# Kernel optimization log

Measured on AMD Instinct MI355X. Metric: run time of the kernel, lower is better.

Reference implementation:

```python
import jax, jax.numpy as jnp
import numpy as np

IMG_H, IMG_W = 512, 512
FEAT_HW = [64, 32, 16, 8, 4]
STRIDES = [8, 16, 32, 64, 128]
IN_CH = 256
NUM_ANCHORS = 9
NUM_CLASSES = 91
SCORE_THRESH = 0.05
NMS_THRESH = 0.5
TOPK = 1000            # batch_size_per_image
DETS = 300             # detections_per_image
BBOX_CLIP = float(np.log(1000.0 / 16.0))
PRIOR_P = 0.01


def _make_anchors():
    # torchvision-style grid anchors, 3 scales x 3 aspect ratios per location
    all_a = []
    for lvl, (hw, stride) in enumerate(zip(FEAT_HW, STRIDES)):
        base = 32.0 * (2.0 ** lvl)
        scales = np.array([1.0, 2.0 ** (1.0 / 3.0), 2.0 ** (2.0 / 3.0)])
        ratios = np.array([0.5, 1.0, 2.0])
        ws = (base * scales[None, :] / np.sqrt(ratios)[:, None]).reshape(-1)  # [9]
        hs = (base * scales[None, :] * np.sqrt(ratios)[:, None]).reshape(-1)
        shifts = (np.arange(hw) + 0.5) * stride
        cy, cx = np.meshgrid(shifts, shifts, indexing='ij')
        cx = cx.reshape(-1, 1)
        cy = cy.reshape(-1, 1)
        a = np.stack([cx - ws / 2, cy - hs / 2, cx + ws / 2, cy + hs / 2], axis=-1)  # [HW, 9, 4]
        all_a.append(a.reshape(-1, 4))
    return np.concatenate(all_a, axis=0).astype(np.float32)


def setup_inputs() -> dict:
    key = jax.random.key(0)
    ks = jax.random.split(key, 10)
    inp = {}
    for i, hw in enumerate(FEAT_HW):
        inp[f'feat{i}'] = jax.random.normal(ks[i], (1, IN_CH, hw, hw), jnp.float32)
    inp['anchors'] = jnp.asarray(_make_anchors())
    tower_std, out_std = 0.03, 0.01
    inp['cls_tower_w'] = jax.random.normal(ks[5], (4, IN_CH, IN_CH, 3, 3), jnp.float32) * tower_std
    inp['cls_tower_b'] = jnp.zeros((4, IN_CH), jnp.float32)
    inp['cls_logits_w'] = jax.random.normal(ks[6], (NUM_ANCHORS * NUM_CLASSES, IN_CH, 3, 3), jnp.float32) * out_std
    inp['cls_logits_b'] = jnp.full((NUM_ANCHORS * NUM_CLASSES,), -np.log((1.0 - PRIOR_P) / PRIOR_P), jnp.float32)
    inp['reg_tower_w'] = jax.random.normal(ks[7], (4, IN_CH, IN_CH, 3, 3), jnp.float32) * tower_std
    inp['reg_tower_b'] = jnp.zeros((4, IN_CH), jnp.float32)
    inp['reg_bbox_w'] = jax.random.normal(ks[8], (NUM_ANCHORS * 4, IN_CH, 3, 3), jnp.float32) * out_std
    inp['reg_bbox_b'] = jnp.zeros((NUM_ANCHORS * 4,), jnp.float32)
    return inp


def _conv3x3(x, w, b):
    y = jax.lax.conv_general_dilated(x, w, (1, 1), 'SAME', dimension_numbers=('NCHW', 'OIHW', 'NCHW'))
    return y + b[None, :, None, None]


def _head(x, tw, tb, ow, ob, out_ch):
    # 4-layer conv tower with ReLU, then output conv; reshape to [B, H*W*A, out_ch]
    for i in range(4):
        x = jax.nn.relu(_conv3x3(x, tw[i], tb[i]))
    y = _conv3x3(x, ow, ob)  # [B, A*out_ch, H, W]
    B, _, H, W = y.shape
    return y.reshape(B, NUM_ANCHORS, out_ch, H, W).transpose(0, 3, 4, 1, 2).reshape(B, H * W * NUM_ANCHORS, out_ch)


def _decode(rel, anc):
    # BoxCoder.decode_single with weights (1,1,1,1)
    w = anc[:, 2] - anc[:, 0]
    h = anc[:, 3] - anc[:, 1]
    cx = anc[:, 0] + 0.5 * w
    cy = anc[:, 1] + 0.5 * h
    dx, dy = rel[:, 0], rel[:, 1]
    dw = jnp.minimum(rel[:, 2], BBOX_CLIP)
    dh = jnp.minimum(rel[:, 3], BBOX_CLIP)
    pcx = dx * w + cx
    pcy = dy * h + cy
    pw = jnp.exp(dw) * w
    ph = jnp.exp(dh) * h
    return jnp.stack([pcx - 0.5 * pw, pcy - 0.5 * ph, pcx + 0.5 * pw, pcy + 0.5 * ph], axis=1)


def _level_candidates(logits, reg, anc):
    # logits [A_l, K], reg [A_l, 4], anc [A_l, 4]
    scores = jax.nn.sigmoid(logits).reshape(-1)          # [A_l*K]
    masked = jnp.where(scores > SCORE_THRESH, scores, -1.0)
    top_s, top_i = jax.lax.top_k(masked, TOPK)           # fixed-size topk; invalid -> -1
    labels = top_i % NUM_CLASSES
    a_idx = top_i // NUM_CLASSES
    boxes = _decode(reg[a_idx], anc[a_idx])
    boxes = jnp.stack([
        jnp.clip(boxes[:, 0], 0.0, float(IMG_W)), jnp.clip(boxes[:, 1], 0.0, float(IMG_H)),
        jnp.clip(boxes[:, 2], 0.0, float(IMG_W)), jnp.clip(boxes[:, 3], 0.0, float(IMG_H))], axis=1)
    return top_s, boxes, labels


def _nms_image(boxes, scores, labels):
    # batched_nms: offset boxes by label so different classes never overlap,
    # then greedy NMS with fixed DETS iterations (padded with invalid slots).
    NEG = jnp.float32(-1e9)
    off = labels.astype(boxes.dtype) * (jnp.max(boxes) + 1.0)
    b = boxes + off[:, None]
    area = (b[:, 2] - b[:, 0]) * (b[:, 3] - b[:, 1])
    alive0 = jnp.where(scores > SCORE_THRESH, scores, NEG)

    def step(alive, _):
        j = jnp.argmax(alive)
        valid = alive[j] > SCORE_THRESH
        bj = b[j]
        lt = jnp.maximum(bj[:2], b[:, :2])
        rb = jnp.minimum(bj[2:], b[:, 2:])
        wh = jnp.maximum(rb - lt, 0.0)
        inter = wh[:, 0] * wh[:, 1]
        iou = inter / (area[j] + area - inter + 1e-12)
        alive = jnp.where(iou > NMS_THRESH, NEG, alive).at[j].set(NEG)
        return alive, (j, valid)

    _, (sel, valid) = jax.lax.scan(step, alive0, None, length=DETS)
    out_s = jnp.where(valid, scores[sel], 0.0)
    out_b = jnp.where(valid[:, None], boxes[sel], 0.0)
    out_l = jnp.where(valid, labels[sel], -1)
    return out_s, out_b, out_l


def _forward(feats, anchors, ctw, ctb, cow, cob, rtw, rtb, row, rob):
    cand = []
    a_off = 0
    for f in feats:
        B, _, H, W = f.shape
        logits = _head(f, ctw, ctb, cow, cob, NUM_CLASSES)   # [B, HWA, K]
        reg = _head(f, rtw, rtb, row, rob, 4)                # [B, HWA, 4]
        a_l = H * W * NUM_ANCHORS
        anc = anchors[a_off:a_off + a_l]
        a_off += a_l
        cand.append(jax.vmap(_level_candidates, in_axes=(0, 0, None))(logits, reg, anc))
    scores = jnp.concatenate([c[0] for c in cand], axis=1)   # [B, 5*TOPK]
    boxes = jnp.concatenate([c[1] for c in cand], axis=1)    # [B, 5*TOPK, 4]
    labels = jnp.concatenate([c[2] for c in cand], axis=1)
    out_s, out_b, out_l = jax.vmap(_nms_image)(boxes, scores, labels)
    out = jnp.concatenate([out_s[..., None], out_b], axis=-1)  # [B, DETS, 5] = (score, x1, y1, x2, y2)
    return out, out_l


def reference(feat0, feat1, feat2, feat3, feat4, anchors, cls_tower_w, cls_tower_b,
              cls_logits_w, cls_logits_b, reg_tower_w, reg_tower_b, reg_bbox_w, reg_bbox_b):
    out, labels = _forward([feat0, feat1, feat2, feat3, feat4], anchors,
                           cls_tower_w, cls_tower_b, cls_logits_w, cls_logits_b,
                           reg_tower_w, reg_tower_b, reg_bbox_w, reg_bbox_b)
    return out, labels
```

## Files before the change

kernel.cpp:

```cpp
#include <hip/hip_runtime.h>
#include <hip/hip_bf16.h>
#include <math.h>

#define CIN 256
#define NUM_CLASSES 91
#define NUM_ANCH 9
#define KEY_CAP 65536
#define NCAND 5000
#define BBOX_CLIP_F 4.135166556742356f
#define CLS_THRESH 0.05f
#define PITCH 5456
#define PP_TOT 5972
#define PLANE_E 1528832
#define PLANE_B 3057664
#define ABUF_B  6115328
#define SLB     147456
#define LO_OFF  13312
#define PHASE   26624

typedef __attribute__((ext_vector_type(4))) float f4;
typedef _Float16 h8 __attribute__((ext_vector_type(8)));

#define MFMA(a,b,c) __builtin_amdgcn_mfma_f32_16x16x32_f16(a,b,c,0,0,0)

__constant__ int c_wsh[5]  = {6,5,4,3,2};
__constant__ int c_hw[5]   = {4096,1024,256,64,16};
__constant__ int c_wp[5]   = {66,34,18,10,6};
__constant__ int c_poff[5] = {0,4356,5512,5836,5936};
__constant__ int c_slen[5] = {198,136,108,100,36};
__constant__ int c_loff[5] = {0,4096,5120,5376,5440};
__constant__ int c_aoff[5] = {0,36864,46080,48384,48960};
__constant__ int s_cum[11] = {0,16,32,48,64,80,96,112,164,168,184};

__device__ __forceinline__ unsigned short f16r(float f) {
    _Float16 h = (_Float16)f;
    return __builtin_bit_cast(unsigned short, h);
}
__device__ __forceinline__ float f16tof(unsigned short u) {
    return (float)__builtin_bit_cast(_Float16, u);
}
__device__ __forceinline__ void split16(float v, unsigned short& h, unsigned short& l) {
    unsigned short hh = (fabsf(v) < 6.103515625e-05f) ? (unsigned short)0 : f16r(v);
    h = hh;
    l = f16r((v - f16tof(hh)) * 4096.0f);
}
__device__ __forceinline__ void gl_lds(const void* g, void* l) {
    __builtin_amdgcn_global_load_lds((const __attribute__((address_space(1))) void*)g,
                                     (__attribute__((address_space(3))) void*)l, 16, 0, 0);
}
__device__ __forceinline__ void tile_geom(int tile, int& lvl, int& px0, int& y0) {
    if (tile < 64)      { lvl = 0; px0 = tile << 6; y0 = tile; }
    else if (tile < 80) { lvl = 1; int j = tile - 64; px0 = j << 6; y0 = j << 1; }
    else if (tile < 84) { lvl = 2; int j = tile - 80; px0 = j << 6; y0 = j << 2; }
    else if (tile == 84){ lvl = 3; px0 = 0; y0 = 0; }
    else                { lvl = 4; px0 = 0; y0 = 0; }
}

__global__ void pad_k(const float* __restrict__ f0, const float* __restrict__ f1,
                      const float* __restrict__ f2, const float* __restrict__ f3,
                      const float* __restrict__ f4, unsigned short* __restrict__ IN) {
    int gid = blockIdx.x * 256 + threadIdx.x;
    if (gid >= 256 * PITCH) return;
    int cin = gid / PITCH, g = gid - cin * PITCH;
    int lvl = (g < 4096) ? 0 : (g < 5120) ? 1 : (g < 5376) ? 2 : (g < 5440) ? 3 : 4;
    const float* f = (lvl == 0) ? f0 : (lvl == 1) ? f1 : (lvl == 2) ? f2 : (lvl == 3) ? f3 : f4;
    int pix = g - c_loff[lvl];
    int wsh = c_wsh[lvl];
    int y = pix >> wsh, x = pix & ((1 << wsh) - 1);
    float v = f[(size_t)cin * c_hw[lvl] + pix];
    unsigned short h, l;
    split16(v, h, l);
    size_t idx = ((size_t)(cin >> 5) * PP_TOT + c_poff[lvl] + (size_t)(y + 1) * c_wp[lvl] + x + 1) * 32 + (cin & 31);
    IN[idx] = h;
    IN[PLANE_E + idx] = l;
}

__global__ void wprep_k(const float* __restrict__ ctw, const float* __restrict__ rtw,
                        const float* __restrict__ cow, const float* __restrict__ row_,
                        unsigned short* __restrict__ wf) {
    int gid = blockIdx.x * 256 + threadIdx.x;
    if (gid >= 184 * 72 * 64) return;
    int lane = gid & 63;
    int t = gid >> 6;
    int tap = t % 9;
    int t2 = t / 9;
    int chunk = t2 & 7;
    int cbg = t2 >> 3;
    int r = 0;
#pragma unroll
    for (int i = 1; i <= 10; ++i) if (cbg >= s_cum[i]) r = i;
    int cbl = cbg - s_cum[r];
    const float* src;
    int coutCnt;
    if (r < 3)       { src = ctw + (size_t)(r + 1) * 589824; coutCnt = 256; }
    else if (r < 7)  { src = rtw + (size_t)(r - 3) * 589824; coutCnt = 256; }
    else if (r == 7) { src = cow; coutCnt = 819; }
    else if (r == 8) { src = row_; coutCnt = 36; }
    else             { src = ctw; coutCnt = 256; }
    int cout = cbl * 16 + (lane & 15);
    int q = lane >> 4;
    unsigned short H[8], L[8];
#pragma unroll
    for (int j = 0; j < 8; ++j) {
        int cin = chunk * 32 + q * 8 + j;
        float v = (cout < coutCnt) ? src[((size_t)cout * 256 + cin) * 9 + tap] : 0.0f;
        split16(v, H[j], L[j]);
    }
    size_t off = (size_t)cbg * 73728 + (size_t)(chunk * 9 + tap) * 1024 + (size_t)lane * 8;
#pragma unroll
    for (int j = 0; j < 8; ++j) { wf[off + j] = H[j]; wf[off + 512 + j] = L[j]; }
}

__device__ __forceinline__ void kloop(const unsigned short* __restrict__ src,
        const char* __restrict__ wf0, char* sm, int wid, int lane,
        int s_base, int s_len, int Wp, const int sloc[2], f4 acc1[2][4], f4 acc2[2][4]) {
    const char* wp = wf0 + lane * 16;
    int nc = (s_len * 64 + 1023) >> 10;
    const char* gbase = (const char*)src;
    {
        const char* g = gbase + (size_t)s_base * 64;
        for (int c = wid; c < nc; c += 4) {
            gl_lds(g + (size_t)c * 1024 + (size_t)lane * 16, sm + c * 1024);
            gl_lds(g + PLANE_B + (size_t)c * 1024 + (size_t)lane * 16, sm + LO_OFF + c * 1024);
        }
    }
    __syncthreads();
    for (int chunk = 0; chunk < 8; ++chunk) {
        char* smc = sm + (chunk & 1) * PHASE;
        if (chunk < 7) {
            char* smn = sm + ((chunk & 1) ^ 1) * PHASE;
            const char* g = gbase + ((size_t)(chunk + 1) * PP_TOT + s_base) * 64;
            for (int c = wid; c < nc; c += 4) {
                gl_lds(g + (size_t)c * 1024 + (size_t)lane * 16, smn + c * 1024);
                gl_lds(g + PLANE_B + (size_t)c * 1024 + (size_t)lane * 16, smn + LO_OFF + c * 1024);
            }
        }
#pragma unroll
        for (int tap = 0; tap < 9; ++tap) {
            int toff = ((tap / 3) - 1) * Wp + (tap % 3) - 1;
            int so = toff * 64;
            int wo = (chunk * 9 + tap) * 2048;
            h8 ah0 = *(const h8*)(smc + sloc[0] + so);
            h8 al0 = *(const h8*)(smc + LO_OFF + sloc[0] + so);
            h8 ah1 = *(const h8*)(smc + sloc[1] + so);
            h8 al1 = *(const h8*)(smc + LO_OFF + sloc[1] + so);
#pragma unroll
            for (int sl = 0; sl < 4; ++sl) {
                h8 bh = *(const h8*)(wp + (size_t)sl * SLB + wo);
                h8 bl = *(const h8*)(wp + (size_t)sl * SLB + wo + 1024);
                acc1[0][sl] = MFMA(ah0, bh, acc1[0][sl]);
                acc2[0][sl] = MFMA(al0, bh, acc2[0][sl]);
                acc2[0][sl] = MFMA(ah0, bl, acc2[0][sl]);
                acc1[1][sl] = MFMA(ah1, bh, acc1[1][sl]);
                acc2[1][sl] = MFMA(al1, bh, acc2[1][sl]);
                acc2[1][sl] = MFMA(ah1, bl, acc2[1][sl]);
            }
        }
        __syncthreads();
    }
}

__global__ __launch_bounds__(256, 3) void conv_t(
        const unsigned short* __restrict__ srcC, const unsigned short* __restrict__ srcR,
        unsigned short* __restrict__ dstC, unsigned short* __restrict__ dstR,
        const unsigned short* __restrict__ wfC, const unsigned short* __restrict__ wfR,
        const float* __restrict__ bC, const float* __restrict__ bR) {
    __shared__ __align__(16) char sm[2 * PHASE];
    int tid = threadIdx.x, lane = tid & 63, wid = tid >> 6;
    int quad = lane >> 4, l16 = lane & 15;
    int bx = blockIdx.x, tile = bx >> 2, rem = bx & 3;
    int tower = rem >> 1, cb = rem & 1;
    const unsigned short* src = tower ? srcR : srcC;
    unsigned short* dst = tower ? dstR : dstC;
    const unsigned short* wfx = tower ? wfR : wfC;
    const float* bias = tower ? bR : bC;

    int lvl, px0, y0;
    tile_geom(tile, lvl, px0, y0);
    int wsh = c_wsh[lvl], HW = c_hw[lvl], Wp = c_wp[lvl];
    int poff = c_poff[lvl];
    int s_base = poff + y0 * Wp, s_len = c_slen[lvl];
    int Mh = (wid & 1) * 32, Nh64 = wid >> 1;

    int sloc[2];
#pragma unroll
    for (int mb = 0; mb < 2; ++mb) {
        int p = px0 + Mh + mb * 16 + l16;
        if (p >= HW) p = HW - 1;
        int y = p >> wsh, x = p & ((1 << wsh) - 1);
        sloc[mb] = ((y - y0 + 1) * Wp + x + 1) * 64 + quad * 16;
    }
    f4 acc1[2][4], acc2[2][4];
#pragma unroll
    for (int mb = 0; mb < 2; ++mb)
#pragma unroll
        for (int sl = 0; sl < 4; ++sl) { acc1[mb][sl] = (f4)0.0f; acc2[mb][sl] = (f4)0.0f; }

    const char* wf0 = (const char*)wfx + (size_t)(cb * 8 + Nh64 * 4) * SLB;
    kloop(src, wf0, sm, wid, lane, s_base, s_len, Wp, sloc, acc1, acc2);

    int cbase = cb * 128 + Nh64 * 64;
    float bv[4];
#pragma unroll
    for (int sl = 0; sl < 4; ++sl) bv[sl] = bias[cbase + sl * 16 + l16];
#pragma unroll
    for (int mb = 0; mb < 2; ++mb) {
        int pb = px0 + Mh + mb * 16 + quad * 4;
#pragma unroll
        for (int r = 0; r < 4; ++r) {
            int p = pb + r;
            bool valid = p < HW;
            int pc = valid ? p : 0;
            int y = pc >> wsh, x = pc & ((1 << wsh) - 1);
            size_t ppix = poff + (size_t)(y + 1) * Wp + x + 1;
#pragma unroll
            for (int sl = 0; sl < 4; ++sl) {
                int coutg = cbase + sl * 16 + l16;
                float v = fmaf(acc2[mb][sl][r], 0.000244140625f, acc1[mb][sl][r]) + bv[sl];
                v = fmaxf(v, 0.0f);
                unsigned short h, l;
                split16(v, h, l);
                size_t idx = ((size_t)(coutg >> 5) * PP_TOT + ppix) * 32 + (coutg & 31);
                if (valid) { dst[idx] = h; dst[PLANE_E + idx] = l; }
            }
        }
    }
}

__global__ __launch_bounds__(256, 3) void mhead_t(
        const unsigned short* __restrict__ srcC, const unsigned short* __restrict__ srcR,
        const unsigned short* __restrict__ wfCls, const unsigned short* __restrict__ wfReg,
        const float* __restrict__ cob, const float* __restrict__ rob,
        unsigned long long* __restrict__ keys, int* __restrict__ cnt,
        float* __restrict__ regout) {
    __shared__ __align__(16) char sm[2 * PHASE];
    int tid = threadIdx.x, lane = tid & 63, wid = tid >> 6;
    int quad = lane >> 4, l16 = lane & 15;
    int bx = blockIdx.x, tile = bx >> 3, sub = bx & 7;
    bool isCls = sub < 7;

    int lvl, px0, y0;
    tile_geom(tile, lvl, px0, y0);
    int wsh = c_wsh[lvl], HW = c_hw[lvl], Wp = c_wp[lvl];
    int poff = c_poff[lvl];
    int s_base = poff + y0 * Wp, s_len = c_slen[lvl];
    int Mh = (wid & 1) * 32, Nh64 = wid >> 1;

    int sloc[2];
#pragma unroll
    for (int mb = 0; mb < 2; ++mb) {
        int p = px0 + Mh + mb * 16 + l16;
        if (p >= HW) p = HW - 1;
        int y = p >> wsh, x = p & ((1 << wsh) - 1);
        sloc[mb] = ((y - y0 + 1) * Wp + x + 1) * 64 + quad * 16;
    }
    f4 acc1[2][4], acc2[2][4];
#pragma unroll
    for (int mb = 0; mb < 2; ++mb)
#pragma unroll
        for (int sl = 0; sl < 4; ++sl) { acc1[mb][sl] = (f4)0.0f; acc2[mb][sl] = (f4)0.0f; }

    const unsigned short* src = isCls ? srcC : srcR;
    const char* wf0 = isCls ? (const char*)wfCls + (size_t)(sub * 8 + Nh64 * 4) * SLB
                            : (const char*)wfReg + (size_t)(Nh64 * 4) * SLB;
    kloop(src, wf0, sm, wid, lane, s_base, s_len, Wp, sloc, acc1, acc2);

    if (isCls) {
        int chb = sub * 128 + Nh64 * 64;
        float cbv[4];
#pragma unroll
        for (int sl = 0; sl < 4; ++sl) {
            int ch = chb + sl * 16 + l16;
            cbv[sl] = (ch < 819) ? cob[ch] : 0.0f;
        }
#pragma unroll
        for (int mb = 0; mb < 2; ++mb) {
            int pb = px0 + Mh + mb * 16 + quad * 4;
#pragma unroll
            for (int r = 0; r < 4; ++r) {
                int p = pb + r;
                bool valid = p < HW;
#pragma unroll
                for (int sl = 0; sl < 4; ++sl) {
                    int ch = chb + sl * 16 + l16;
                    if (valid && ch < 819) {
                        float lg = fmaf(acc2[mb][sl][r], 0.000244140625f, acc1[mb][sl][r]) + cbv[sl];
                        float s = 1.0f / (1.0f + expf(-lg));
                        if (s > CLS_THRESH) {
                            int a = ch / NUM_CLASSES;
                            int cls = ch - a * NUM_CLASSES;
                            unsigned flat = (unsigned)((p * NUM_ANCH + a) * NUM_CLASSES + cls);
                            int pos = atomicAdd(cnt + lvl, 1);
                            if (pos < KEY_CAP)
                                keys[(size_t)lvl * KEY_CAP + pos] =
                                    ((unsigned long long)__float_as_uint(s) << 32) |
                                    (unsigned long long)(~flat);
                        }
                    }
                }
            }
        }
    } else {
        int chb = Nh64 * 64;
        float rbv[4];
#pragma unroll
        for (int sl = 0; sl < 4; ++sl) {
            int ch = chb + sl * 16 + l16;
            rbv[sl] = (ch < 36) ? rob[ch] : 0.0f;
        }
        int loff = c_loff[lvl];
#pragma unroll
        for (int mb = 0; mb < 2; ++mb) {
            int pb = px0 + Mh + mb * 16 + quad * 4;
#pragma unroll
            for (int r = 0; r < 4; ++r) {
                int p = pb + r;
                bool valid = p < HW;
#pragma unroll
                for (int sl = 0; sl < 4; ++sl) {
                    int ch = chb + sl * 16 + l16;
                    if (valid && ch < 36)
                        regout[(size_t)ch * PITCH + loff + p] =
                            fmaf(acc2[mb][sl][r], 0.000244140625f, acc1[mb][sl][r]) + rbv[sl];
                }
            }
        }
    }
}

__global__ __launch_bounds__(1024) void sort5_k(unsigned long long* keys, const int* cnt) {
    const int lvl = blockIdx.x;
    unsigned long long* kb = keys + (size_t)lvl * KEY_CAP;
    int n = cnt[lvl]; if (n > KEY_CAP) n = KEY_CAP;
    int m = 2; while (m < n) m <<= 1;
    __shared__ unsigned long long sk[8192];
    if (m <= 8192) {
        for (int i = threadIdx.x; i < m; i += 1024) sk[i] = (i < n) ? kb[i] : 0ull;
        __syncthreads();
        for (int k = 2; k <= m; k <<= 1)
            for (int j = k >> 1; j > 0; j >>= 1) {
                for (int i = threadIdx.x; i < m; i += 1024) {
                    int ixj = i ^ j;
                    if (ixj > i) {
                        unsigned long long a = sk[i], b = sk[ixj];
                        bool desc = (i & k) == 0;
                        if (desc ? (a < b) : (a > b)) { sk[i] = b; sk[ixj] = a; }
                    }
                }
                __syncthreads();
            }
        for (int i = threadIdx.x; i < m; i += 1024) kb[i] = sk[i];
    } else {
        for (int i = threadIdx.x; i < m; i += 1024) if (i >= n) kb[i] = 0ull;
        __syncthreads();
        for (int k = 2; k <= m; k <<= 1)
            for (int j = k >> 1; j > 0; j >>= 1) {
                for (int i = threadIdx.x; i < m; i += 1024) {
                    int ixj = i ^ j;
                    if (ixj > i) {
                        unsigned long long a = kb[i], b = kb[ixj];
                        bool desc = (i & k) == 0;
                        if (desc ? (a < b) : (a > b)) { kb[i] = b; kb[ixj] = a; }
                    }
                }
                __syncthreads();
            }
    }
}

__global__ void emit_k(const unsigned long long* __restrict__ keys, const int* __restrict__ cnt,
                       const float* __restrict__ regout, const float* __restrict__ anchors,
                       float* __restrict__ cs, float* __restrict__ cb, int* __restrict__ cl) {
#pragma clang fp contract(off)
    int r = blockIdx.x * 256 + threadIdx.x;
    if (r >= NCAND) return;
    int lvl = r / 1000, rr = r - lvl * 1000;
    int n = cnt[lvl]; if (n > KEY_CAP) n = KEY_CAP; if (n > 1000) n = 1000;
    float score = -1.0f, b0 = 0.f, b1 = 0.f, b2 = 0.f, b3 = 0.f;
    int label = 0;
    if (rr < n) {
        unsigned long long key = keys[(size_t)lvl * KEY_CAP + rr];
        score = __uint_as_float((unsigned)(key >> 32));
        unsigned flat = ~((unsigned)(key & 0xFFFFFFFFull));
        label = (int)(flat % NUM_CLASSES);
        int af = (int)(flat / NUM_CLASSES);
        int a = af % NUM_ANCH;
        int pix = af / NUM_ANCH;
        int gp = c_loff[lvl] + pix;
        float dx = regout[(size_t)(a * 4 + 0) * PITCH + gp];
        float dy = regout[(size_t)(a * 4 + 1) * PITCH + gp];
        float dw = regout[(size_t)(a * 4 + 2) * PITCH + gp];
        float dh = regout[(size_t)(a * 4 + 3) * PITCH + gp];
        const float* an = anchors + (size_t)(c_aoff[lvl] + af) * 4;
        float aw = an[2] - an[0];
        float ah = an[3] - an[1];
        float cx = an[0] + 0.5f * aw;
        float cy = an[1] + 0.5f * ah;
        dw = fminf(dw, BBOX_CLIP_F);
        dh = fminf(dh, BBOX_CLIP_F);
        float pcx = dx * aw + cx;
        float pcy = dy * ah + cy;
        float pw = expf(dw) * aw;
        float ph = expf(dh) * ah;
        b0 = fminf(fmaxf(pcx - 0.5f * pw, 0.0f), 512.0f);
        b1 = fminf(fmaxf(pcy - 0.5f * ph, 0.0f), 512.0f);
        b2 = fminf(fmaxf(pcx + 0.5f * pw, 0.0f), 512.0f);
        b3 = fminf(fmaxf(pcy + 0.5f * ph, 0.0f), 512.0f);
    }
    cs[r] = score;
    cb[(size_t)r * 4 + 0] = b0;
    cb[(size_t)r * 4 + 1] = b1;
    cb[(size_t)r * 4 + 2] = b2;
    cb[(size_t)r * 4 + 3] = b3;
    cl[r] = label;
}

__global__ void rank_k(const float* __restrict__ cs, const float* __restrict__ cbx,
                       const int* __restrict__ cl, const int* __restrict__ cnt,
                       int* __restrict__ order, float* __restrict__ sbox,
                       float* __restrict__ sarea, int* __restrict__ nvp) {
#pragma clang fp contract(off)
    __shared__ int vls[5];
    int t = blockIdx.x * 256 + threadIdx.x;
    if (threadIdx.x < 5) {
        int n = cnt[threadIdx.x]; if (n > 1000) n = 1000;
        vls[threadIdx.x] = n;
    }
    __syncthreads();
    if (t >= NCAND) return;
    if (t == 0) *nvp = vls[0] + vls[1] + vls[2] + vls[3] + vls[4];
    int lvl = t / 1000, pos = t - lvl * 1000;
    if (pos >= vls[lvl]) return;
    float s = cs[t];
    int rank = pos;
#pragma unroll
    for (int l2 = 0; l2 < 5; ++l2) {
        if (l2 == lvl) continue;
        int n = vls[l2];
        const float* seg = cs + l2 * 1000;
        int lo = 0, hi = n;
        if (l2 < lvl) {
            while (lo < hi) { int mid = (lo + hi) >> 1; if (seg[mid] >= s) lo = mid + 1; else hi = mid; }
        } else {
            while (lo < hi) { int mid = (lo + hi) >> 1; if (seg[mid] > s) lo = mid + 1; else hi = mid; }
        }
        rank += lo;
    }
    order[rank] = t;
    float off = (float)cl[t] * 513.0f;
    float x1 = cbx[(size_t)t * 4 + 0] + off;
    float y1 = cbx[(size_t)t * 4 + 1] + off;
    float x2 = cbx[(size_t)t * 4 + 2] + off;
    float y2 = cbx[(size_t)t * 4 + 3] + off;
    sbox[(size_t)rank * 4 + 0] = x1;
    sbox[(size_t)rank * 4 + 1] = y1;
    sbox[(size_t)rank * 4 + 2] = x2;
    sbox[(size_t)rank * 4 + 3] = y2;
    sarea[rank] = (x2 - x1) * (y2 - y1);
}

__global__ void mask_k(const float* __restrict__ sbox, const float* __restrict__ sarea,
                       const int* __restrict__ nvp, unsigned long long* __restrict__ mask) {
#pragma clang fp contract(off)
    int nv = *nvp;
    int t = blockIdx.x * 256 + threadIdx.x;
    if (t >= NCAND * 80) return;
    int i = t / 80, w = t - i * 80;
    if (i >= nv) return;
    float ix1 = sbox[(size_t)i * 4 + 0];
    float iy1 = sbox[(size_t)i * 4 + 1];
    float ix2 = sbox[(size_t)i * 4 + 2];
    float iy2 = sbox[(size_t)i * 4 + 3];
    float ai = sarea[i];
    unsigned long long bits = 0ull;
    int j0 = w * 64;
    for (int b = 0; b < 64; ++b) {
        int j = j0 + b;
        if (j < nv) {
            float jx1 = sbox[(size_t)j * 4 + 0];
            float jy1 = sbox[(size_t)j * 4 + 1];
            float jx2 = sbox[(size_t)j * 4 + 2];
            float jy2 = sbox[(size_t)j * 4 + 3];
            float aj = sarea[j];
            float ltx = fmaxf(ix1, jx1), lty = fmaxf(iy1, jy1);
            float rbx = fminf(ix2, jx2), rby = fminf(iy2, jy2);
            float wx = fmaxf(rbx - ltx, 0.0f), wy = fmaxf(rby - lty, 0.0f);
            float inter = wx * wy;
            float iou = inter / (ai + aj - inter + 1e-12f);
            if (iou > 0.5f) bits |= (1ull << b);
        }
    }
    mask[(size_t)i * 80 + w] = bits;
}

__global__ __launch_bounds__(64) void sweep_k(const unsigned long long* __restrict__ mask,
        const int* __restrict__ nvp, int* __restrict__ accbuf, int* __restrict__ naccp) {
    const int l = threadIdx.x;
    int nv = *nvp; if (nv > NCAND) nv = NCAND;
    int nacc = 0;
    if (nv > 0) {
        unsigned long long sup0 = 0ull, sup1 = 0ull;
        int ntiles = (nv + 63) >> 6;
        bool done = false;
        for (int g0 = 0; g0 < ntiles && !done; g0 += 8) {
            int gcnt = ntiles - g0; if (gcnt > 8) gcnt = 8;
            unsigned long long ml[8];
#pragma unroll
            for (int g = 0; g < 8; ++g) {
                int t = g0 + g;
                int row = (t << 6) + l;
                ml[g] = (g < gcnt && row < nv) ? mask[(size_t)row * 80 + t] : 0ull;
            }
            for (int g = 0; g < gcnt && !done; ++g) {
                int t = g0 + g;
                unsigned long long cur = (t < 64)
                    ? (unsigned long long)__shfl((long long)sup0, t, 64)
                    : (unsigned long long)__shfl((long long)sup1, t - 64, 64);
                int lim = nv - (t << 6);
                unsigned long long valid = (lim >= 64) ? ~0ull : ((1ull << lim) - 1ull);
                unsigned long long rem = ~cur & valid;
                unsigned long long Aset = 0ull;
                while (rem) {
                    int k = __builtin_ctzll(rem);
                    Aset |= 1ull << k;
                    if (l == 0) accbuf[nacc] = (t << 6) + k;
                    ++nacc;
                    if (nacc == 300) { done = true; break; }
                    unsigned long long mlk = (unsigned long long)__shfl((long long)ml[g], k, 64);
                    cur |= mlk | (1ull << k);
                    rem = ~cur & valid;
                }
                if (!done) {
                    unsigned long long t2 = Aset;
                    while (t2) {
                        int i0 = __builtin_ctzll(t2); t2 &= t2 - 1;
                        int i1 = -1, i2 = -1, i3 = -1;
                        if (t2) { i1 = __builtin_ctzll(t2); t2 &= t2 - 1; }
                        if (t2) { i2 = __builtin_ctzll(t2); t2 &= t2 - 1; }
                        if (t2) { i3 = __builtin_ctzll(t2); t2 &= t2 - 1; }
                        size_t r0 = (size_t)((t << 6) + i0) * 80;
                        unsigned long long w0 = mask[r0 + l];
                        unsigned long long w1 = (i1 >= 0) ? mask[(size_t)((t << 6) + i1) * 80 + l] : 0ull;
                        unsigned long long w2 = (i2 >= 0) ? mask[(size_t)((t << 6) + i2) * 80 + l] : 0ull;
                        unsigned long long w3 = (i3 >= 0) ? mask[(size_t)((t << 6) + i3) * 80 + l] : 0ull;
                        sup0 |= w0 | w1 | w2 | w3;
                        if (l < 16) {
                            unsigned long long v0 = mask[r0 + 64 + l];
                            unsigned long long v1 = (i1 >= 0) ? mask[(size_t)((t << 6) + i1) * 80 + 64 + l] : 0ull;
                            unsigned long long v2 = (i2 >= 0) ? mask[(size_t)((t << 6) + i2) * 80 + 64 + l] : 0ull;
                            unsigned long long v3 = (i3 >= 0) ? mask[(size_t)((t << 6) + i3) * 80 + 64 + l] : 0ull;
                            sup1 |= v0 | v1 | v2 | v3;
                        }
                    }
                }
            }
        }
    }
    if (l == 0) *naccp = nacc;
}

__global__ void fill_k(const float* __restrict__ cs, const float* __restrict__ cb,
                       const int* __restrict__ cl, const int* __restrict__ order,
                       const int* __restrict__ accbuf, const int* __restrict__ naccp,
                       float* __restrict__ out) {
    int t = blockIdx.x * 64 + threadIdx.x;
    if (t >= 300) return;
    int na = *naccp;
    if (t < na) {
        int c = order[accbuf[t]];
        out[t * 5 + 0] = cs[c];
        out[t * 5 + 1] = cb[(size_t)c * 4 + 0];
        out[t * 5 + 2] = cb[(size_t)c * 4 + 1];
        out[t * 5 + 3] = cb[(size_t)c * 4 + 2];
        out[t * 5 + 4] = cb[(size_t)c * 4 + 3];
        out[1500 + t] = (float)cl[c];
    } else {
        out[t * 5 + 0] = 0.0f; out[t * 5 + 1] = 0.0f; out[t * 5 + 2] = 0.0f;
        out[t * 5 + 3] = 0.0f; out[t * 5 + 4] = 0.0f;
        out[1500 + t] = -1.0f;
    }
}

extern "C" void kernel_launch(void* const* d_in, const int* in_sizes, int n_in,
                              void* d_out, int out_size, void* d_ws, size_t ws_size,
                              hipStream_t stream) {
    const float* f0 = (const float*)d_in[0];
    const float* f1 = (const float*)d_in[1];
    const float* f2 = (const float*)d_in[2];
    const float* f3 = (const float*)d_in[3];
    const float* f4 = (const float*)d_in[4];
    const float* anchors = (const float*)d_in[5];
    const float* ctw = (const float*)d_in[6];
    const float* ctb = (const float*)d_in[7];
    const float* cow = (const float*)d_in[8];
    const float* cob = (const float*)d_in[9];
    const float* rtw = (const float*)d_in[10];
    const float* rtb = (const float*)d_in[11];
    const float* row_ = (const float*)d_in[12];
    const float* rob = (const float*)d_in[13];
    float* out = (float*)d_out;

    char* base = (char*)d_ws;
    unsigned short* wf = (unsigned short*)base;
    unsigned short* C  = (unsigned short*)(base + 24772608);
    unsigned short* IN = (unsigned short*)(base + 30887936);
    unsigned short* A  = (unsigned short*)(base + 37003264);
    unsigned short* B  = (unsigned short*)(base + 43118592);
    int* cnt           = (int*)(base + 49233920);
    int* nvp           = cnt + 6;
    int* naccp         = cnt + 7;
    float* cs    = (float*)(base + 0);
    float* cbx   = (float*)(base + 32768);
    int*   cl    = (int*)(base + 131072);
    int*   order = (int*)(base + 163840);
    float* sbox  = (float*)(base + 262144);
    float* sarea = (float*)(base + 344064);
    int*   accbuf = (int*)(base + 368640);
    unsigned long long* keys = (unsigned long long*)A;
    float* regout            = (float*)(base + 37003264 + 2621440);
    unsigned long long* mask = (unsigned long long*)B;

    unsigned short* SL_clsL[4] = {wf + (size_t)168 * 73728, wf + (size_t)0 * 73728,
                                  wf + (size_t)16 * 73728,  wf + (size_t)32 * 73728};
    unsigned short* SL_regL[4] = {wf + (size_t)48 * 73728, wf + (size_t)64 * 73728,
                                  wf + (size_t)80 * 73728, wf + (size_t)96 * 73728};
    unsigned short* SL_clsH = wf + (size_t)112 * 73728;
    unsigned short* SL_regH = wf + (size_t)164 * 73728;

    hipMemsetAsync(C, 0, 4 * (size_t)ABUF_B, stream);
    hipMemsetAsync(cnt, 0, 32, stream);

    pad_k<<<(256 * PITCH + 255) / 256, 256, 0, stream>>>(f0, f1, f2, f3, f4, IN);
    wprep_k<<<(184 * 72 * 64 + 255) / 256, 256, 0, stream>>>(ctw, rtw, cow, row_, wf);

    conv_t<<<86 * 4, 256, 0, stream>>>(IN, IN, A, B, SL_clsL[0], SL_regL[0], ctb, rtb);
    hipMemsetAsync(C, 0, (size_t)ABUF_B, stream);
    conv_t<<<86 * 4, 256, 0, stream>>>(A, B, C, IN, SL_clsL[1], SL_regL[1], ctb + 256, rtb + 256);
    conv_t<<<86 * 4, 256, 0, stream>>>(C, IN, A, B, SL_clsL[2], SL_regL[2], ctb + 512, rtb + 512);
    conv_t<<<86 * 4, 256, 0, stream>>>(A, B, C, IN, SL_clsL[3], SL_regL[3], ctb + 768, rtb + 768);

    mhead_t<<<86 * 8, 256, 0, stream>>>(C, IN, SL_clsH, SL_regH, cob, rob, keys, cnt, regout);

    sort5_k<<<5, 1024, 0, stream>>>(keys, cnt);
    emit_k<<<(NCAND + 255) / 256, 256, 0, stream>>>(keys, cnt, regout, anchors, cs, cbx, cl);
    rank_k<<<(NCAND + 255) / 256, 256, 0, stream>>>(cs, cbx, cl, cnt, order, sbox, sarea, nvp);
    mask_k<<<(NCAND * 80 + 255) / 256, 256, 0, stream>>>(sbox, sarea, nvp, mask);
    sweep_k<<<1, 64, 0, stream>>>(mask, nvp, accbuf, naccp);
    fill_k<<<5, 64, 0, stream>>>(cs, cbx, cl, order, accbuf, naccp, out);
}
```

Before: 653.2 us.

## Halve output-channel tile per block, double grid, prefetch weight fragments across taps

Each conv and head block now covers 64 output channels instead of 128, with each wave holding 2 channel slices instead of 4. This doubles the conv grid and expands the head grid to 14 blocks per tile, which raises parallelism and cuts accumulator registers. The tap loop also software-pipelines the B-fragment global loads, issuing the next tap's weights before the current tap's MFMAs to hide latency. The cost is that every input tile is staged into LDS twice as often per output channel, which doubles activation traffic per unit of MFMA work.

After: 528.2 us. 1.24x faster.

```diff
diff --git a/kernel.cpp b/kernel.cpp
--- a/kernel.cpp
+++ b/kernel.cpp
@@ -113,7 +113,7 @@
 
 __device__ __forceinline__ void kloop(const unsigned short* __restrict__ src,
         const char* __restrict__ wf0, char* sm, int wid, int lane,
-        int s_base, int s_len, int Wp, const int sloc[2], f4 acc1[2][4], f4 acc2[2][4]) {
+        int s_base, int s_len, int Wp, const int sloc[2], f4 acc1[2][2], f4 acc2[2][2]) {
     const char* wp = wf0 + lane * 16;
     int nc = (s_len * 64 + 1023) >> 10;
     const char* gbase = (const char*)src;
@@ -124,6 +124,10 @@
             gl_lds(g + PLANE_B + (size_t)c * 1024 + (size_t)lane * 16, sm + LO_OFF + c * 1024);
         }
     }
+    h8 bh0 = *(const h8*)(wp);
+    h8 bl0 = *(const h8*)(wp + 1024);
+    h8 bh1 = *(const h8*)(wp + SLB);
+    h8 bl1 = *(const h8*)(wp + SLB + 1024);
     __syncthreads();
     for (int chunk = 0; chunk < 8; ++chunk) {
         char* smc = sm + (chunk & 1) * PHASE;
@@ -137,24 +141,31 @@
         }
 #pragma unroll
         for (int tap = 0; tap < 9; ++tap) {
+            int kt = chunk * 9 + tap;
+            int wo2 = ((kt < 71) ? kt + 1 : kt) * 2048;
+            h8 nh0 = *(const h8*)(wp + wo2);
+            h8 nl0 = *(const h8*)(wp + wo2 + 1024);
+            h8 nh1 = *(const h8*)(wp + SLB + wo2);
+            h8 nl1 = *(const h8*)(wp + SLB + wo2 + 1024);
             int toff = ((tap / 3) - 1) * Wp + (tap % 3) - 1;
             int so = toff * 64;
-            int wo = (chunk * 9 + tap) * 2048;
             h8 ah0 = *(const h8*)(smc + sloc[0] + so);
             h8 al0 = *(const h8*)(smc + LO_OFF + sloc[0] + so);
             h8 ah1 = *(const h8*)(smc + sloc[1] + so);
             h8 al1 = *(const h8*)(smc + LO_OFF + sloc[1] + so);
-#pragma unroll
-            for (int sl = 0; sl < 4; ++sl) {
-                h8 bh = *(const h8*)(wp + (size_t)sl * SLB + wo);
-                h8 bl = *(const h8*)(wp + (size_t)sl * SLB + wo + 1024);
-                acc1[0][sl] = MFMA(ah0, bh, acc1[0][sl]);
-                acc2[0][sl] = MFMA(al0, bh, acc2[0][sl]);
-                acc2[0][sl] = MFMA(ah0, bl, acc2[0][sl]);
-                acc1[1][sl] = MFMA(ah1, bh, acc1[1][sl]);
-                acc2[1][sl] = MFMA(al1, bh, acc2[1][sl]);
-                acc2[1][sl] = MFMA(ah1, bl, acc2[1][sl]);
-            }
+            acc1[0][0] = MFMA(ah0, bh0, acc1[0][0]);
+            acc2[0][0] = MFMA(al0, bh0, acc2[0][0]);
+            acc2[0][0] = MFMA(ah0, bl0, acc2[0][0]);
+            acc1[1][0] = MFMA(ah1, bh0, acc1[1][0]);
+            acc2[1][0] = MFMA(al1, bh0, acc2[1][0]);
+            acc2[1][0] = MFMA(ah1, bl0, acc2[1][0]);
+            acc1[0][1] = MFMA(ah0, bh1, acc1[0][1]);
+            acc2[0][1] = MFMA(al0, bh1, acc2[0][1]);
+            acc2[0][1] = MFMA(ah0, bl1, acc2[0][1]);
+            acc1[1][1] = MFMA(ah1, bh1, acc1[1][1]);
+            acc2[1][1] = MFMA(al1, bh1, acc2[1][1]);
+            acc2[1][1] = MFMA(ah1, bl1, acc2[1][1]);
+            bh0 = nh0; bl0 = nl0; bh1 = nh1; bl1 = nl1;
         }
         __syncthreads();
     }
@@ -168,8 +179,8 @@
     __shared__ __align__(16) char sm[2 * PHASE];
     int tid = threadIdx.x, lane = tid & 63, wid = tid >> 6;
     int quad = lane >> 4, l16 = lane & 15;
-    int bx = blockIdx.x, tile = bx >> 2, rem = bx & 3;
-    int tower = rem >> 1, cb = rem & 1;
+    int bx = blockIdx.x;
+    int cb = bx & 3, tower = (bx >> 2) & 1, tile = bx >> 3;
     const unsigned short* src = tower ? srcR : srcC;
     unsigned short* dst = tower ? dstR : dstC;
     const unsigned short* wfx = tower ? wfR : wfC;
@@ -180,7 +191,7 @@
     int wsh = c_wsh[lvl], HW = c_hw[lvl], Wp = c_wp[lvl];
     int poff = c_poff[lvl];
     int s_base = poff + y0 * Wp, s_len = c_slen[lvl];
-    int Mh = (wid & 1) * 32, Nh64 = wid >> 1;
+    int Mh = (wid & 1) * 32, Nh32 = wid >> 1;
 
     int sloc[2];
 #pragma unroll
@@ -190,19 +201,19 @@
         int y = p >> wsh, x = p & ((1 << wsh) - 1);
         sloc[mb] = ((y - y0 + 1) * Wp + x + 1) * 64 + quad * 16;
     }
-    f4 acc1[2][4], acc2[2][4];
+    f4 acc1[2][2], acc2[2][2];
 #pragma unroll
     for (int mb = 0; mb < 2; ++mb)
 #pragma unroll
-        for (int sl = 0; sl < 4; ++sl) { acc1[mb][sl] = (f4)0.0f; acc2[mb][sl] = (f4)0.0f; }
-
-    const char* wf0 = (const char*)wfx + (size_t)(cb * 8 + Nh64 * 4) * SLB;
+        for (int sl = 0; sl < 2; ++sl) { acc1[mb][sl] = (f4)0.0f; acc2[mb][sl] = (f4)0.0f; }
+
+    const char* wf0 = (const char*)wfx + (size_t)(cb * 4 + Nh32 * 2) * SLB;
     kloop(src, wf0, sm, wid, lane, s_base, s_len, Wp, sloc, acc1, acc2);
 
-    int cbase = cb * 128 + Nh64 * 64;
-    float bv[4];
-#pragma unroll
-    for (int sl = 0; sl < 4; ++sl) bv[sl] = bias[cbase + sl * 16 + l16];
+    int cbase = cb * 64 + Nh32 * 32;
+    float bv[2];
+    bv[0] = bias[cbase + l16];
+    bv[1] = bias[cbase + 16 + l16];
 #pragma unroll
     for (int mb = 0; mb < 2; ++mb) {
         int pb = px0 + Mh + mb * 16 + quad * 4;
@@ -214,7 +225,7 @@
             int y = pc >> wsh, x = pc & ((1 << wsh) - 1);
             size_t ppix = poff + (size_t)(y + 1) * Wp + x + 1;
 #pragma unroll
-            for (int sl = 0; sl < 4; ++sl) {
+            for (int sl = 0; sl < 2; ++sl) {
                 int coutg = cbase + sl * 16 + l16;
                 float v = fmaf(acc2[mb][sl][r], 0.000244140625f, acc1[mb][sl][r]) + bv[sl];
                 v = fmaxf(v, 0.0f);
@@ -236,15 +247,15 @@
     __shared__ __align__(16) char sm[2 * PHASE];
     int tid = threadIdx.x, lane = tid & 63, wid = tid >> 6;
     int quad = lane >> 4, l16 = lane & 15;
-    int bx = blockIdx.x, tile = bx >> 3, sub = bx & 7;
-    bool isCls = sub < 7;
+    int bx = blockIdx.x, tile = bx / 14, sub = bx - tile * 14;
+    bool isCls = sub < 13;
 
     int lvl, px0, y0;
     tile_geom(tile, lvl, px0, y0);
     int wsh = c_wsh[lvl], HW = c_hw[lvl], Wp = c_wp[lvl];
     int poff = c_poff[lvl];
     int s_base = poff + y0 * Wp, s_len = c_slen[lvl];
-    int Mh = (wid & 1) * 32, Nh64 = wid >> 1;
+    int Mh = (wid & 1) * 32, Nh32 = wid >> 1;
 
     int sloc[2];
 #pragma unroll
@@ -254,22 +265,22 @@
         int y = p >> wsh, x = p & ((1 << wsh) - 1);
         sloc[mb] = ((y - y0 + 1) * Wp + x + 1) * 64 + quad * 16;
     }
-    f4 acc1[2][4], acc2[2][4];
+    f4 acc1[2][2], acc2[2][2];
 #pragma unroll
     for (int mb = 0; mb < 2; ++mb)
 #pragma unroll
-        for (int sl = 0; sl < 4; ++sl) { acc1[mb][sl] = (f4)0.0f; acc2[mb][sl] = (f4)0.0f; }
+        for (int sl = 0; sl < 2; ++sl) { acc1[mb][sl] = (f4)0.0f; acc2[mb][sl] = (f4)0.0f; }
 
     const unsigned short* src = isCls ? srcC : srcR;
-    const char* wf0 = isCls ? (const char*)wfCls + (size_t)(sub * 8 + Nh64 * 4) * SLB
-                            : (const char*)wfReg + (size_t)(Nh64 * 4) * SLB;
+    const char* wf0 = isCls ? (const char*)wfCls + (size_t)(sub * 4 + Nh32 * 2) * SLB
+                            : (const char*)wfReg + (size_t)(Nh32 * 2) * SLB;
     kloop(src, wf0, sm, wid, lane, s_base, s_len, Wp, sloc, acc1, acc2);
 
     if (isCls) {
-        int chb = sub * 128 + Nh64 * 64;
-        float cbv[4];
-#pragma unroll
-        for (int sl = 0; sl < 4; ++sl) {
+        int chb = sub * 64 + Nh32 * 32;
+        float cbv[2];
+#pragma unroll
+        for (int sl = 0; sl < 2; ++sl) {
             int ch = chb + sl * 16 + l16;
             cbv[sl] = (ch < 819) ? cob[ch] : 0.0f;
         }
@@ -281,7 +292,7 @@
                 int p = pb + r;
                 bool valid = p < HW;
 #pragma unroll
-                for (int sl = 0; sl < 4; ++sl) {
+                for (int sl = 0; sl < 2; ++sl) {
                     int ch = chb + sl * 16 + l16;
                     if (valid && ch < 819) {
                         float lg = fmaf(acc2[mb][sl][r], 0.000244140625f, acc1[mb][sl][r]) + cbv[sl];
@@ -301,10 +312,10 @@
             }
         }
     } else {
-        int chb = Nh64 * 64;
-        float rbv[4];
-#pragma unroll
-        for (int sl = 0; sl < 4; ++sl) {
+        int chb = Nh32 * 32;
+        float rbv[2];
+#pragma unroll
+        for (int sl = 0; sl < 2; ++sl) {
             int ch = chb + sl * 16 + l16;
             rbv[sl] = (ch < 36) ? rob[ch] : 0.0f;
         }
@@ -317,7 +328,7 @@
                 int p = pb + r;
                 bool valid = p < HW;
 #pragma unroll
-                for (int sl = 0; sl < 4; ++sl) {
+                for (int sl = 0; sl < 2; ++sl) {
                     int ch = chb + sl * 16 + l16;
                     if (valid && ch < 36)
                         regout[(size_t)ch * PITCH + loff + p] =
@@ -633,13 +644,13 @@
     pad_k<<<(256 * PITCH + 255) / 256, 256, 0, stream>>>(f0, f1, f2, f3, f4, IN);
     wprep_k<<<(184 * 72 * 64 + 255) / 256, 256, 0, stream>>>(ctw, rtw, cow, row_, wf);
 
-    conv_t<<<86 * 4, 256, 0, stream>>>(IN, IN, A, B, SL_clsL[0], SL_regL[0], ctb, rtb);
+    conv_t<<<86 * 8, 256, 0, stream>>>(IN, IN, A, B, SL_clsL[0], SL_regL[0], ctb, rtb);
     hipMemsetAsync(C, 0, (size_t)ABUF_B, stream);
-    conv_t<<<86 * 4, 256, 0, stream>>>(A, B, C, IN, SL_clsL[1], SL_regL[1], ctb + 256, rtb + 256);
-    conv_t<<<86 * 4, 256, 0, stream>>>(C, IN, A, B, SL_clsL[2], SL_regL[2], ctb + 512, rtb + 512);
-    conv_t<<<86 * 4, 256, 0, stream>>>(A, B, C, IN, SL_clsL[3], SL_regL[3], ctb + 768, rtb + 768);
-
-    mhead_t<<<86 * 8, 256, 0, stream>>>(C, IN, SL_clsH, SL_regH, cob, rob, keys, cnt, regout);
+    conv_t<<<86 * 8, 256, 0, stream>>>(A, B, C, IN, SL_clsL[1], SL_regL[1], ctb + 256, rtb + 256);
+    conv_t<<<86 * 8, 256, 0, stream>>>(C, IN, A, B, SL_clsL[2], SL_regL[2], ctb + 512, rtb + 512);
+    conv_t<<<86 * 8, 256, 0, stream>>>(A, B, C, IN, SL_clsL[3], SL_regL[3], ctb + 768, rtb + 768);
+
+    mhead_t<<<86 * 14, 256, 0, stream>>>(C, IN, SL_clsH, SL_regH, cob, rob, keys, cnt, regout);
 
     sort5_k<<<5, 1024, 0, stream>>>(keys, cnt);
     emit_k<<<(NCAND + 255) / 256, 256, 0, stream>>>(keys, cnt, regout, anchors, cs, cbx, cl);
```

## Halve conv blocks to two waves, swizzle activation layout, prefetch weights

Applied to the files above, without the earlier changes.

Conv and head kernels now run 128-thread blocks, two waves each covering 32 pixels by 64 output channels. This doubles the grid, so each block handles 64 channels instead of 128. The activation layout in global and LDS memory gains an XOR swizzle of the 8-channel groups keyed on pixel index, meant to reduce LDS bank conflicts on the A-operand reads. Weight fragments are loaded one tap ahead in registers to hide global latency. The cost is that each activation tile is staged into LDS twice as often across blocks, and register pressure rises.

New measurement: 680.3 us. 1.04x slower.

```diff
diff --git a/kernel.cpp b/kernel.cpp
--- a/kernel.cpp
+++ b/kernel.cpp
@@ -70,7 +70,10 @@
     float v = f[(size_t)cin * c_hw[lvl] + pix];
     unsigned short h, l;
     split16(v, h, l);
-    size_t idx = ((size_t)(cin >> 5) * PP_TOT + c_poff[lvl] + (size_t)(y + 1) * c_wp[lvl] + x + 1) * 32 + (cin & 31);
+    size_t ppix = c_poff[lvl] + (size_t)(y + 1) * c_wp[lvl] + x + 1;
+    int qc = (cin >> 3) & 3;
+    size_t idx = ((size_t)(cin >> 5) * PP_TOT + ppix) * 32 +
+                 (size_t)((qc ^ ((int)ppix & 3)) << 3) + (cin & 7);
     IN[idx] = h;
     IN[PLANE_E + idx] = l;
 }
@@ -112,55 +115,73 @@
 }
 
 __device__ __forceinline__ void kloop(const unsigned short* __restrict__ src,
-        const char* __restrict__ wf0, char* sm, int wid, int lane,
-        int s_base, int s_len, int Wp, const int sloc[2], f4 acc1[2][4], f4 acc2[2][4]) {
+        const char* __restrict__ wf0, char* sm, int wid, int lane, int quad,
+        int s_base, int s_len, int Wp, const int relrow[2], f4 acc1[2][4], f4 acc2[2][4]) {
     const char* wp = wf0 + lane * 16;
     int nc = (s_len * 64 + 1023) >> 10;
     const char* gbase = (const char*)src;
     {
         const char* g = gbase + (size_t)s_base * 64;
-        for (int c = wid; c < nc; c += 4) {
+        for (int c = wid; c < nc; c += 2) {
             gl_lds(g + (size_t)c * 1024 + (size_t)lane * 16, sm + c * 1024);
             gl_lds(g + PLANE_B + (size_t)c * 1024 + (size_t)lane * 16, sm + LO_OFF + c * 1024);
         }
     }
+    h8 bh[4], bl[4];
+#pragma unroll
+    for (int sl = 0; sl < 4; ++sl) {
+        bh[sl] = *(const h8*)(wp + (size_t)sl * SLB);
+        bl[sl] = *(const h8*)(wp + (size_t)sl * SLB + 1024);
+    }
     __syncthreads();
+    int qsh = quad << 4;
     for (int chunk = 0; chunk < 8; ++chunk) {
         char* smc = sm + (chunk & 1) * PHASE;
         if (chunk < 7) {
             char* smn = sm + ((chunk & 1) ^ 1) * PHASE;
             const char* g = gbase + ((size_t)(chunk + 1) * PP_TOT + s_base) * 64;
-            for (int c = wid; c < nc; c += 4) {
+            for (int c = wid; c < nc; c += 2) {
                 gl_lds(g + (size_t)c * 1024 + (size_t)lane * 16, smn + c * 1024);
                 gl_lds(g + PLANE_B + (size_t)c * 1024 + (size_t)lane * 16, smn + LO_OFF + c * 1024);
             }
         }
 #pragma unroll
         for (int tap = 0; tap < 9; ++tap) {
+            int kt = chunk * 9 + tap;
+            int wo2 = ((kt < 71) ? kt + 1 : kt) * 2048;
+            h8 nh[4], nl[4];
+#pragma unroll
+            for (int sl = 0; sl < 4; ++sl) {
+                nh[sl] = *(const h8*)(wp + (size_t)sl * SLB + wo2);
+                nl[sl] = *(const h8*)(wp + (size_t)sl * SLB + wo2 + 1024);
+            }
             int toff = ((tap / 3) - 1) * Wp + (tap % 3) - 1;
-            int so = toff * 64;
-            int wo = (chunk * 9 + tap) * 2048;
-            h8 ah0 = *(const h8*)(smc + sloc[0] + so);
-            h8 al0 = *(const h8*)(smc + LO_OFF + sloc[0] + so);
-            h8 ah1 = *(const h8*)(smc + sloc[1] + so);
-            h8 al1 = *(const h8*)(smc + LO_OFF + sloc[1] + so);
+            h8 ah[2], al[2];
+#pragma unroll
+            for (int mb = 0; mb < 2; ++mb) {
+                int arow = relrow[mb] + toff;
+                int sw = qsh ^ (((s_base + arow) & 3) << 4);
+                int addr = arow * 64 + sw;
+                ah[mb] = *(const h8*)(smc + addr);
+                al[mb] = *(const h8*)(smc + LO_OFF + addr);
+            }
 #pragma unroll
             for (int sl = 0; sl < 4; ++sl) {
-                h8 bh = *(const h8*)(wp + (size_t)sl * SLB + wo);
-                h8 bl = *(const h8*)(wp + (size_t)sl * SLB + wo + 1024);
-                acc1[0][sl] = MFMA(ah0, bh, acc1[0][sl]);
-                acc2[0][sl] = MFMA(al0, bh, acc2[0][sl]);
-                acc2[0][sl] = MFMA(ah0, bl, acc2[0][sl]);
-                acc1[1][sl] = MFMA(ah1, bh, acc1[1][sl]);
-                acc2[1][sl] = MFMA(al1, bh, acc2[1][sl]);
-                acc2[1][sl] = MFMA(ah1, bl, acc2[1][sl]);
-            }
+                acc1[0][sl] = MFMA(ah[0], bh[sl], acc1[0][sl]);
+                acc2[0][sl] = MFMA(al[0], bh[sl], acc2[0][sl]);
+                acc2[0][sl] = MFMA(ah[0], bl[sl], acc2[0][sl]);
+                acc1[1][sl] = MFMA(ah[1], bh[sl], acc1[1][sl]);
+                acc2[1][sl] = MFMA(al[1], bh[sl], acc2[1][sl]);
+                acc2[1][sl] = MFMA(ah[1], bl[sl], acc2[1][sl]);
+            }
+#pragma unroll
+            for (int sl = 0; sl < 4; ++sl) { bh[sl] = nh[sl]; bl[sl] = nl[sl]; }
         }
         __syncthreads();
     }
 }
 
-__global__ __launch_bounds__(256, 3) void conv_t(
+__global__ __launch_bounds__(128, 2) void conv_t(
         const unsigned short* __restrict__ srcC, const unsigned short* __restrict__ srcR,
         unsigned short* __restrict__ dstC, unsigned short* __restrict__ dstR,
         const unsigned short* __restrict__ wfC, const unsigned short* __restrict__ wfR,
@@ -168,8 +189,8 @@
     __shared__ __align__(16) char sm[2 * PHASE];
     int tid = threadIdx.x, lane = tid & 63, wid = tid >> 6;
     int quad = lane >> 4, l16 = lane & 15;
-    int bx = blockIdx.x, tile = bx >> 2, rem = bx & 3;
-    int tower = rem >> 1, cb = rem & 1;
+    int bx = blockIdx.x;
+    int cb = bx & 3, tower = (bx >> 2) & 1, tile = bx >> 3;
     const unsigned short* src = tower ? srcR : srcC;
     unsigned short* dst = tower ? dstR : dstC;
     const unsigned short* wfx = tower ? wfR : wfC;
@@ -180,15 +201,15 @@
     int wsh = c_wsh[lvl], HW = c_hw[lvl], Wp = c_wp[lvl];
     int poff = c_poff[lvl];
     int s_base = poff + y0 * Wp, s_len = c_slen[lvl];
-    int Mh = (wid & 1) * 32, Nh64 = wid >> 1;
-
-    int sloc[2];
+    int Mh = wid * 32;
+
+    int relrow[2];
 #pragma unroll
     for (int mb = 0; mb < 2; ++mb) {
         int p = px0 + Mh + mb * 16 + l16;
         if (p >= HW) p = HW - 1;
         int y = p >> wsh, x = p & ((1 << wsh) - 1);
-        sloc[mb] = ((y - y0 + 1) * Wp + x + 1) * 64 + quad * 16;
+        relrow[mb] = (y - y0 + 1) * Wp + x + 1;
     }
     f4 acc1[2][4], acc2[2][4];
 #pragma unroll
@@ -196,10 +217,10 @@
 #pragma unroll
         for (int sl = 0; sl < 4; ++sl) { acc1[mb][sl] = (f4)0.0f; acc2[mb][sl] = (f4)0.0f; }
 
-    const char* wf0 = (const char*)wfx + (size_t)(cb * 8 + Nh64 * 4) * SLB;
-    kloop(src, wf0, sm, wid, lane, s_base, s_len, Wp, sloc, acc1, acc2);
-
-    int cbase = cb * 128 + Nh64 * 64;
+    const char* wf0 = (const char*)wfx + (size_t)(cb * 4) * SLB;
+    kloop(src, wf0, sm, wid, lane, quad, s_base, s_len, Wp, relrow, acc1, acc2);
+
+    int cbase = cb * 64;
     float bv[4];
 #pragma unroll
     for (int sl = 0; sl < 4; ++sl) bv[sl] = bias[cbase + sl * 16 + l16];
@@ -220,14 +241,16 @@
                 v = fmaxf(v, 0.0f);
                 unsigned short h, l;
                 split16(v, h, l);
-                size_t idx = ((size_t)(coutg >> 5) * PP_TOT + ppix) * 32 + (coutg & 31);
+                int c31 = coutg & 31;
+                size_t idx = ((size_t)(coutg >> 5) * PP_TOT + ppix) * 32 +
+                             (size_t)(((c31 >> 3) ^ ((int)ppix & 3)) << 3) + (c31 & 7);
                 if (valid) { dst[idx] = h; dst[PLANE_E + idx] = l; }
             }
         }
     }
 }
 
-__global__ __launch_bounds__(256, 3) void mhead_t(
+__global__ __launch_bounds__(128, 2) void mhead_t(
         const unsigned short* __restrict__ srcC, const unsigned short* __restrict__ srcR,
         const unsigned short* __restrict__ wfCls, const unsigned short* __restrict__ wfReg,
         const float* __restrict__ cob, const float* __restrict__ rob,
@@ -236,23 +259,23 @@
     __shared__ __align__(16) char sm[2 * PHASE];
     int tid = threadIdx.x, lane = tid & 63, wid = tid >> 6;
     int quad = lane >> 4, l16 = lane & 15;
-    int bx = blockIdx.x, tile = bx >> 3, sub = bx & 7;
-    bool isCls = sub < 7;
+    int bx = blockIdx.x, tile = bx / 14, sub = bx - tile * 14;
+    bool isCls = sub < 13;
 
     int lvl, px0, y0;
     tile_geom(tile, lvl, px0, y0);
     int wsh = c_wsh[lvl], HW = c_hw[lvl], Wp = c_wp[lvl];
     int poff = c_poff[lvl];
     int s_base = poff + y0 * Wp, s_len = c_slen[lvl];
-    int Mh = (wid & 1) * 32, Nh64 = wid >> 1;
-
-    int sloc[2];
+    int Mh = wid * 32;
+
+    int relrow[2];
 #pragma unroll
     for (int mb = 0; mb < 2; ++mb) {
         int p = px0 + Mh + mb * 16 + l16;
         if (p >= HW) p = HW - 1;
         int y = p >> wsh, x = p & ((1 << wsh) - 1);
-        sloc[mb] = ((y - y0 + 1) * Wp + x + 1) * 64 + quad * 16;
+        relrow[mb] = (y - y0 + 1) * Wp + x + 1;
     }
     f4 acc1[2][4], acc2[2][4];
 #pragma unroll
@@ -261,12 +284,12 @@
         for (int sl = 0; sl < 4; ++sl) { acc1[mb][sl] = (f4)0.0f; acc2[mb][sl] = (f4)0.0f; }
 
     const unsigned short* src = isCls ? srcC : srcR;
-    const char* wf0 = isCls ? (const char*)wfCls + (size_t)(sub * 8 + Nh64 * 4) * SLB
-                            : (const char*)wfReg + (size_t)(Nh64 * 4) * SLB;
-    kloop(src, wf0, sm, wid, lane, s_base, s_len, Wp, sloc, acc1, acc2);
+    const char* wf0 = isCls ? (const char*)wfCls + (size_t)(sub * 4) * SLB
+                            : (const char*)wfReg;
+    kloop(src, wf0, sm, wid, lane, quad, s_base, s_len, Wp, relrow, acc1, acc2);
 
     if (isCls) {
-        int chb = sub * 128 + Nh64 * 64;
+        int chb = sub * 64;
         float cbv[4];
 #pragma unroll
         for (int sl = 0; sl < 4; ++sl) {
@@ -301,11 +324,10 @@
             }
         }
     } else {
-        int chb = Nh64 * 64;
         float rbv[4];
 #pragma unroll
         for (int sl = 0; sl < 4; ++sl) {
-            int ch = chb + sl * 16 + l16;
+            int ch = sl * 16 + l16;
             rbv[sl] = (ch < 36) ? rob[ch] : 0.0f;
         }
         int loff = c_loff[lvl];
@@ -318,7 +340,7 @@
                 bool valid = p < HW;
 #pragma unroll
                 for (int sl = 0; sl < 4; ++sl) {
-                    int ch = chb + sl * 16 + l16;
+                    int ch = sl * 16 + l16;
                     if (valid && ch < 36)
                         regout[(size_t)ch * PITCH + loff + p] =
                             fmaf(acc2[mb][sl][r], 0.000244140625f, acc1[mb][sl][r]) + rbv[sl];
@@ -633,13 +655,13 @@
     pad_k<<<(256 * PITCH + 255) / 256, 256, 0, stream>>>(f0, f1, f2, f3, f4, IN);
     wprep_k<<<(184 * 72 * 64 + 255) / 256, 256, 0, stream>>>(ctw, rtw, cow, row_, wf);
 
-    conv_t<<<86 * 4, 256, 0, stream>>>(IN, IN, A, B, SL_clsL[0], SL_regL[0], ctb, rtb);
+    conv_t<<<86 * 8, 128, 0, stream>>>(IN, IN, A, B, SL_clsL[0], SL_regL[0], ctb, rtb);
     hipMemsetAsync(C, 0, (size_t)ABUF_B, stream);
-    conv_t<<<86 * 4, 256, 0, stream>>>(A, B, C, IN, SL_clsL[1], SL_regL[1], ctb + 256, rtb + 256);
-    conv_t<<<86 * 4, 256, 0, stream>>>(C, IN, A, B, SL_clsL[2], SL_regL[2], ctb + 512, rtb + 512);
-    conv_t<<<86 * 4, 256, 0, stream>>>(A, B, C, IN, SL_clsL[3], SL_regL[3], ctb + 768, rtb + 768);
-
-    mhead_t<<<86 * 8, 256, 0, stream>>>(C, IN, SL_clsH, SL_regH, cob, rob, keys, cnt, regout);
+    conv_t<<<86 * 8, 128, 0, stream>>>(A, B, C, IN, SL_clsL[1], SL_regL[1], ctb + 256, rtb + 256);
+    conv_t<<<86 * 8, 128, 0, stream>>>(C, IN, A, B, SL_clsL[2], SL_regL[2], ctb + 512, rtb + 512);
+    conv_t<<<86 * 8, 128, 0, stream>>>(A, B, C, IN, SL_clsL[3], SL_regL[3], ctb + 768, rtb + 768);
+
+    mhead_t<<<86 * 14, 128, 0, stream>>>(C, IN, SL_clsH, SL_regH, cob, rob, keys, cnt, regout);
 
     sort5_k<<<5, 1024, 0, stream>>>(keys, cnt);
     emit_k<<<(NCAND + 255) / 256, 256, 0, stream>>>(keys, cnt, regout, anchors, cs, cbx, cl);
```
